# Optimization experiments

Measured on AMD Instinct MI355X. Metric: run time of the kernel, lower is better.

## Reference

```python
import jax, jax.numpy as jnp
import numpy as np

SHIFTS = (1, 2, 4, 8)  # exponential strategy, num_shifts=4

B, L, D = 2, 2048, 2048
CAT = D * (1 + 2 * len(SHIFTS))  # 18432


def setup_inputs() -> dict:
    key = jax.random.key(0)
    kx, kw, kb = jax.random.split(key, 3)
    x = jax.random.normal(kx, (B, L, D), dtype=jnp.float32)
    # nn.Linear(cat_dim, dim_out) weight is [dim_out, cat_dim]; store as [cat_dim, dim_out] transposed for matmul
    W = jax.random.normal(kw, (D, CAT), dtype=jnp.float32) * (1.0 / np.sqrt(CAT))
    b = jax.random.normal(kb, (D,), dtype=jnp.float32) * 0.01
    return {"x": x, "W": W, "b": b}


def reference(x, W, b):
    # x: [B, L, D]; W: [dim_out, cat_dim]; b: [dim_out]
    glo = jnp.mean(x, axis=1, keepdims=True)  # [B, 1, D] global context
    feats = [jax.nn.silu(x)]
    for s in SHIFTS:
        rg = jnp.roll(glo, s, axis=-1)          # [B, 1, D]
        xg = x * rg                              # [B, L, D]
        feats.append(jax.nn.silu(xg))            # inner(s)
        rx = jnp.roll(x, s, axis=-1)
        feats.append(xg - rx * glo)              # wedge(s)
    mixed = jnp.concatenate(feats, axis=-1)      # [B, L, cat_dim]
    out = jnp.einsum('blc,oc->blo', mixed, W) + b
    return out
```

## Files before the change

kernel.cpp:

```cpp
#include <hip/hip_runtime.h>
#include <stdint.h>

#define DDIM 2048
#define LDIM 2048
#define BDIM 2
#define CATK 18432
#define MDIM 4096
#define NDIM 2048
#define KGEMM 12288
#define KCHUNK 6144

typedef short bf16x8 __attribute__((ext_vector_type(8)));
typedef float f32x4 __attribute__((ext_vector_type(4)));
typedef unsigned short u16x8 __attribute__((ext_vector_type(8)));

__device__ __forceinline__ unsigned short f2bf(float f) {
  uint32_t u = __float_as_uint(f);
  return (unsigned short)((u + 0x7fffu + ((u >> 16) & 1u)) >> 16);
}
__device__ __forceinline__ float bf2f(unsigned short h) {
  return __uint_as_float((uint32_t)h << 16);
}
__device__ __forceinline__ float silu_f(float v) { return v / (1.0f + __expf(-v)); }

__device__ __forceinline__ void async16(const void* g, void* l) {
  __builtin_amdgcn_global_load_lds(
      (const __attribute__((address_space(1))) uint32_t*)(uintptr_t)g,
      (__attribute__((address_space(3))) uint32_t*)(uintptr_t)l, 16, 0, 0);
}

__global__ __launch_bounds__(256) void glo_partial(const float* __restrict__ x,
                                                   float* __restrict__ part) {
  int g = blockIdx.x;
  int dc = g & 7, sl = (g >> 3) & 15, b = g >> 7;
  int d = dc * 256 + threadIdx.x;
  const float* p = x + ((size_t)b * LDIM + (size_t)sl * 128) * DDIM + d;
  float s = 0.f;
  #pragma unroll 8
  for (int i = 0; i < 128; ++i) s += p[(size_t)i * DDIM];
  part[(size_t)(b * 16 + sl) * DDIM + d] = s;
}

__global__ __launch_bounds__(256) void glo_final(const float* __restrict__ part,
                                                 float* __restrict__ glo) {
  int idx = blockIdx.x * 256 + threadIdx.x;
  int b = idx >> 11, d = idx & 2047;
  float s = 0.f;
  #pragma unroll
  for (int i = 0; i < 16; ++i) s += part[(size_t)(b * 16 + i) * DDIM + d];
  glo[idx] = s * (1.0f / (float)LDIM);
}

__global__ __launch_bounds__(256) void conv_wB(const float* __restrict__ W,
                                               unsigned short* __restrict__ B0,
                                               unsigned short* __restrict__ B1) {
  int k = blockIdx.x;
  int o = blockIdx.y;
  int srcb = (k == 0) ? 0 : (k == 1) ? 1 : (k == 2) ? 3 : (k == 3) ? 5 : 7;
  const float* src = W + (size_t)o * CATK + srcb * 2048 + threadIdx.x * 8;
  f32x4 a = *(const f32x4*)src;
  f32x4 c = *(const f32x4*)(src + 4);
  u16x8 v;
  v[0] = f2bf(a[0]); v[1] = f2bf(a[1]); v[2] = f2bf(a[2]); v[3] = f2bf(a[3]);
  v[4] = f2bf(c[0]); v[5] = f2bf(c[1]); v[6] = f2bf(c[2]); v[7] = f2bf(c[3]);
  if (k < 3) {
    *(u16x8*)(B0 + (size_t)o * KCHUNK + k * 2048 + threadIdx.x * 8) = v;
  } else {
    size_t d = (size_t)o * KCHUNK + (size_t)(k - 3) * 2048 + threadIdx.x * 8;
    *(u16x8*)(B1 + d) = v;
    *(u16x8*)(B1 + (size_t)2048 * KCHUNK + d) = v;
  }
}

__global__ __launch_bounds__(256) void fold_w(const float* __restrict__ W,
                                              const float* __restrict__ glo,
                                              unsigned short* __restrict__ B1) {
  __shared__ float ws[4][2048];
  __shared__ float g2[2][2048];
  int o = blockIdx.x;
  for (int i = threadIdx.x; i < 512; i += 256) {
    *(f32x4*)&g2[0][i * 4] = *(const f32x4*)&glo[i * 4];
    *(f32x4*)&g2[1][i * 4] = *(const f32x4*)&glo[2048 + i * 4];
    #pragma unroll
    for (int j = 0; j < 4; ++j)
      *(f32x4*)&ws[j][i * 4] =
          *(const f32x4*)(W + (size_t)o * CATK + (2 + 2 * j) * 2048 + i * 4);
  }
  __syncthreads();
  int d0 = threadIdx.x * 8;
  #pragma unroll
  for (int b = 0; b < 2; ++b) {
    u16x8 outv;
    #pragma unroll
    for (int e = 0; e < 8; ++e) {
      int d = d0 + e;
      float v = 0.f;
      #pragma unroll
      for (int j = 0; j < 4; ++j) {
        int s = 1 << j;
        int dm = (d - s) & 2047, dp = (d + s) & 2047;
        v += ws[j][d] * g2[b][dm] - ws[j][dp] * g2[b][dp];
      }
      outv[e] = f2bf(v);
    }
    *(u16x8*)(B1 + (size_t)b * 2048 * KCHUNK + (size_t)o * KCHUNK + 4096 + d0) = outv;
  }
}

__global__ __launch_bounds__(256) void build_mixed(const float* __restrict__ x,
                                                   const float* __restrict__ glo,
                                                   unsigned short* __restrict__ mixed) {
  __shared__ float xs[DDIM];
  __shared__ float gs[DDIM];
  int row = blockIdx.x;
  int b = row >> 11;
  const float* xr = x + (size_t)row * DDIM;
  const float* gr = glo + (size_t)b * DDIM;
  for (int i = threadIdx.x; i < DDIM / 4; i += 256) {
    *(f32x4*)&xs[i * 4] = *(const f32x4*)&xr[i * 4];
    *(f32x4*)&gs[i * 4] = *(const f32x4*)&gr[i * 4];
  }
  __syncthreads();
  unsigned short* mr = mixed + (size_t)row * KGEMM;
  int d0 = threadIdx.x * 8;
  u16x8 o0, oi[4], xb;
  #pragma unroll
  for (int j = 0; j < 8; ++j) {
    int d = d0 + j;
    float xv = xs[d];
    o0[j] = f2bf(silu_f(xv));
    xb[j] = f2bf(xv);
    #pragma unroll
    for (int si = 0; si < 4; ++si) {
      int s = 1 << si;
      int dm = (d - s) & (DDIM - 1);
      oi[si][j] = f2bf(silu_f(xv * gs[dm]));
    }
  }
  *(u16x8*)(mr + d0) = o0;
  #pragma unroll
  for (int si = 0; si < 4; ++si)
    *(u16x8*)(mr + (size_t)(1 + si) * DDIM + d0) = oi[si];
  *(u16x8*)(mr + (size_t)10240 + d0) = xb;
}

#define BAR() __builtin_amdgcn_s_barrier()
#define SCHEDB() __builtin_amdgcn_sched_barrier(0)
#define WAIT_VM4() asm volatile("s_waitcnt vmcnt(4)" ::: "memory")
#define WAIT_VM0() asm volatile("s_waitcnt vmcnt(0)" ::: "memory")
#define WAIT_LGKM0() asm volatile("s_waitcnt lgkmcnt(0)" ::: "memory")

#define STAGE_A(S, H, KREL)                                            \
  do {                                                                 \
    const unsigned short* g_ = gA + (size_t)((H)*128) * KGEMM + (KREL);\
    unsigned short* l_ = stA + ((S)*2 + (H)) * 8192;                   \
    async16(g_, l_);                                                   \
    async16(g_ + (size_t)8 * KGEMM, l_ + 512);                         \
  } while (0)

#define STAGE_B(S, H, KREL)                                             \
  do {                                                                  \
    const unsigned short* g_ = gB + (size_t)((H)*128) * KCHUNK + (KREL);\
    unsigned short* l_ = stB + ((S)*2 + (H)) * 8192;                    \
    async16(g_, l_);                                                    \
    async16(g_ + (size_t)8 * KCHUNK, l_ + 512);                         \
  } while (0)

#define LOAD_A(S, MH)                                                        \
  do {                                                                       \
    _Pragma("unroll") for (int mi = 0; mi < 4; ++mi) {                       \
      ra[mi][0] = *(const bf16x8*)(pA + (S)*16384 + ((MH)*64 + mi*16)*64 + sl0); \
      ra[mi][1] = *(const bf16x8*)(pA + (S)*16384 + ((MH)*64 + mi*16)*64 + sl1); \
    }                                                                        \
  } while (0)

#define LOAD_B(S, NH, RB)                                                    \
  do {                                                                       \
    _Pragma("unroll") for (int nj = 0; nj < 2; ++nj) {                       \
      RB[nj][0] = *(const bf16x8*)(pB + (S)*16384 + ((NH)*32 + nj*16)*64 + sl0); \
      RB[nj][1] = *(const bf16x8*)(pB + (S)*16384 + ((NH)*32 + nj*16)*64 + sl1); \
    }                                                                        \
  } while (0)

#define MFMA_QUAD(MH, NH, RB)                                                \
  do {                                                                       \
    __builtin_amdgcn_s_setprio(1);                                           \
    _Pragma("unroll") for (int kk = 0; kk < 2; ++kk)                         \
      _Pragma("unroll") for (int mi = 0; mi < 4; ++mi)                       \
        _Pragma("unroll") for (int nj = 0; nj < 2; ++nj)                     \
          acc[(MH)*4 + mi][(NH)*2 + nj] = __builtin_amdgcn_mfma_f32_16x16x32_bf16( \
              ra[mi][kk], RB[nj][kk], acc[(MH)*4 + mi][(NH)*2 + nj], 0, 0, 0);     \
    __builtin_amdgcn_s_setprio(0);                                           \
  } while (0)

__global__ __launch_bounds__(512, 2) void gemm256(const unsigned short* __restrict__ A,
                                                  const unsigned short* __restrict__ B0,
                                                  const unsigned short* __restrict__ B1,
                                                  const float* __restrict__ bias,
                                                  unsigned short* __restrict__ P0,
                                                  unsigned short* __restrict__ P1) {
  extern __shared__ unsigned short lds[];
  unsigned short* ldsA = lds;
  unsigned short* ldsB = lds + 32768;

  int bid = blockIdx.x;
  int swz = (bid & 7) * 32 + (bid >> 3);
  int kc = swz >> 7;
  int rem = swz & 127;
  int mt = rem >> 3, nt = rem & 7;
  size_t kbase = (size_t)kc * KCHUNK;

  int tid = threadIdx.x;
  int wave = tid >> 6, lane = tid & 63;
  int wr = wave >> 2, wcol = wave & 3;
  int lrow = lane & 15, kq = lane >> 4, r3 = lrow & 7;
  int rIn8 = lane >> 3;
  int scOff = ((lane & 7) ^ rIn8) * 8;
  int wv16 = wave * 16;

  const unsigned short* gA = A + (size_t)(mt * 256 + wv16 + rIn8) * KGEMM + kbase + scOff;
  const unsigned short* gBb = kc ? (B1 + (size_t)((mt >= 8) ? 2048 : 0) * KCHUNK) : B0;
  const unsigned short* gB = gBb + (size_t)(nt * 256 + wv16 + rIn8) * KCHUNK + scOff;
  unsigned short* stA = ldsA + wv16 * 64;
  unsigned short* stB = ldsB + wv16 * 64;

  const unsigned short* pA = ldsA + wr * 8192 + lrow * 64;
  const unsigned short* pB = ldsB + (wcol >> 1) * 8192 + ((wcol & 1) * 64 + lrow) * 64;
  int sl0 = (kq ^ r3) * 8, sl1 = ((kq + 4) ^ r3) * 8;

  f32x4 acc[8][4];
  #pragma unroll
  for (int i = 0; i < 8; ++i)
    #pragma unroll
    for (int j = 0; j < 4; ++j) acc[i][j] = (f32x4)0.f;
  bf16x8 ra[4][2], rb0[2][2], rb1[2][2];

  STAGE_B(0, 0, 0); STAGE_B(0, 1, 0);
  STAGE_A(0, 0, 0); STAGE_A(0, 1, 0);
  STAGE_B(1, 0, 64); STAGE_B(1, 1, 64);
  WAIT_VM4(); SCHEDB();
  BAR(); SCHEDB();

  for (int t = 0; t < 47; ++t) {
    size_t k0 = (size_t)t * 128;
    LOAD_A(0, 0); LOAD_B(0, 0, rb0);
    STAGE_A(1, 0, k0 + 64);
    BAR(); WAIT_LGKM0(); SCHEDB();
    MFMA_QUAD(0, 0, rb0);
    SCHEDB(); BAR(); SCHEDB();
    LOAD_B(0, 1, rb1);
    STAGE_A(1, 1, k0 + 64);
    BAR(); WAIT_LGKM0(); SCHEDB();
    MFMA_QUAD(0, 1, rb1);
    SCHEDB(); BAR(); SCHEDB();
    LOAD_A(0, 1);
    STAGE_B(0, 0, k0 + 128);
    BAR(); WAIT_LGKM0(); SCHEDB();
    MFMA_QUAD(1, 1, rb1);
    SCHEDB(); BAR(); SCHEDB();
    STAGE_B(0, 1, k0 + 128);
    BAR(); SCHEDB();
    MFMA_QUAD(1, 0, rb0);
    WAIT_VM4(); SCHEDB(); BAR(); SCHEDB();
    LOAD_A(1, 0); LOAD_B(1, 0, rb0);
    STAGE_A(0, 0, k0 + 128);
    BAR(); WAIT_LGKM0(); SCHEDB();
    MFMA_QUAD(0, 0, rb0);
    SCHEDB(); BAR(); SCHEDB();
    LOAD_B(1, 1, rb1);
    STAGE_A(0, 1, k0 + 128);
    BAR(); WAIT_LGKM0(); SCHEDB();
    MFMA_QUAD(0, 1, rb1);
    SCHEDB(); BAR(); SCHEDB();
    LOAD_A(1, 1);
    STAGE_B(1, 0, k0 + 192);
    BAR(); WAIT_LGKM0(); SCHEDB();
    MFMA_QUAD(1, 1, rb1);
    SCHEDB(); BAR(); SCHEDB();
    STAGE_B(1, 1, k0 + 192);
    BAR(); SCHEDB();
    MFMA_QUAD(1, 0, rb0);
    WAIT_VM4(); SCHEDB(); BAR(); SCHEDB();
  }

  {
    size_t k0 = (size_t)47 * 128;
    LOAD_A(0, 0); LOAD_B(0, 0, rb0);
    STAGE_A(1, 0, k0 + 64);
    BAR(); WAIT_LGKM0(); SCHEDB();
    MFMA_QUAD(0, 0, rb0);
    SCHEDB(); BAR(); SCHEDB();
    LOAD_B(0, 1, rb1);
    STAGE_A(1, 1, k0 + 64);
    BAR(); WAIT_LGKM0(); SCHEDB();
    MFMA_QUAD(0, 1, rb1);
    SCHEDB(); BAR(); SCHEDB();
    LOAD_A(0, 1);
    BAR(); WAIT_LGKM0(); SCHEDB();
    MFMA_QUAD(1, 1, rb1);
    SCHEDB(); BAR(); SCHEDB();
    BAR(); SCHEDB();
    MFMA_QUAD(1, 0, rb0);
    WAIT_VM0(); SCHEDB(); BAR(); SCHEDB();
    LOAD_A(1, 0); LOAD_B(1, 0, rb0);
    BAR(); WAIT_LGKM0(); SCHEDB();
    MFMA_QUAD(0, 0, rb0);
    SCHEDB(); BAR(); SCHEDB();
    LOAD_B(1, 1, rb1);
    BAR(); WAIT_LGKM0(); SCHEDB();
    MFMA_QUAD(0, 1, rb1);
    SCHEDB(); BAR(); SCHEDB();
    LOAD_A(1, 1);
    BAR(); WAIT_LGKM0(); SCHEDB();
    MFMA_QUAD(1, 1, rb1);
    SCHEDB(); BAR(); SCHEDB();
    MFMA_QUAD(1, 0, rb0);
  }

  unsigned short* dst = kc ? P1 : P0;
  float bv[4];
  #pragma unroll
  for (int J = 0; J < 4; ++J)
    bv[J] = kc ? 0.f : bias[nt * 256 + wcol * 64 + J * 16 + lrow];
  #pragma unroll
  for (int I = 0; I < 8; ++I) {
    int row0 = mt * 256 + wr * 128 + I * 16 + kq * 4;
    #pragma unroll
    for (int J = 0; J < 4; ++J) {
      int col = nt * 256 + wcol * 64 + J * 16 + lrow;
      #pragma unroll
      for (int r = 0; r < 4; ++r)
        dst[(size_t)(row0 + r) * NDIM + col] = f2bf(acc[I][J][r] + bv[J]);
    }
  }
}

__global__ __launch_bounds__(256) void combine(float* __restrict__ out,
                                               const unsigned short* __restrict__ p0,
                                               const unsigned short* __restrict__ p1) {
  size_t n = (size_t)MDIM * NDIM / 8;
  size_t stride = (size_t)gridDim.x * 256;
  for (size_t i = (size_t)blockIdx.x * 256 + threadIdx.x; i < n; i += stride) {
    u16x8 a = *(const u16x8*)(p0 + i * 8);
    u16x8 c = *(const u16x8*)(p1 + i * 8);
    f32x4 lo, hi;
    #pragma unroll
    for (int j = 0; j < 4; ++j) {
      lo[j] = bf2f(a[j]) + bf2f(c[j]);
      hi[j] = bf2f(a[j + 4]) + bf2f(c[j + 4]);
    }
    *(f32x4*)(out + i * 8) = lo;
    *(f32x4*)(out + i * 8 + 4) = hi;
  }
}

extern "C" void kernel_launch(void* const* d_in, const int* in_sizes, int n_in,
                              void* d_out, int out_size, void* d_ws, size_t ws_size,
                              hipStream_t stream) {
  const float* x = (const float*)d_in[0];
  const float* W = (const float*)d_in[1];
  const float* b = (const float*)d_in[2];
  float* out = (float*)d_out;

  uint8_t* ws = (uint8_t*)d_ws;
  size_t offB0 = 0;
  size_t szB0 = (size_t)NDIM * KCHUNK * 2;
  size_t offB1 = offB0 + szB0;
  size_t szB1 = (size_t)2 * NDIM * KCHUNK * 2;
  size_t offMx = offB1 + szB1;
  size_t szMx = (size_t)MDIM * KGEMM * 2;
  size_t offGlo = offMx + szMx;
  size_t szGlo = (size_t)BDIM * DDIM * 4;
  size_t offPart = offGlo + szGlo;
  size_t szPart = (size_t)BDIM * 16 * DDIM * 4;
  size_t offP0 = offPart + szPart;
  size_t szP0 = (size_t)MDIM * NDIM * 2;
  size_t offP1 = offP0 + szP0;
  size_t szP1 = (size_t)MDIM * NDIM * 2;
  if (ws_size < offP1 + szP1) return;

  unsigned short* B0 = (unsigned short*)(ws + offB0);
  unsigned short* B1 = (unsigned short*)(ws + offB1);
  unsigned short* Mx = (unsigned short*)(ws + offMx);
  float* glo = (float*)(ws + offGlo);
  float* part = (float*)(ws + offPart);
  unsigned short* P0 = (unsigned short*)(ws + offP0);
  unsigned short* P1 = (unsigned short*)(ws + offP1);

  hipFuncSetAttribute((const void*)gemm256, hipFuncAttributeMaxDynamicSharedMemorySize,
                      131072);

  hipLaunchKernelGGL(glo_partial, dim3(256), dim3(256), 0, stream, x, part);
  hipLaunchKernelGGL(glo_final, dim3(16), dim3(256), 0, stream, part, glo);
  hipLaunchKernelGGL(conv_wB, dim3(5, 2048), dim3(256), 0, stream, W, B0, B1);
  hipLaunchKernelGGL(fold_w, dim3(2048), dim3(256), 0, stream, W, glo, B1);
  hipLaunchKernelGGL(build_mixed, dim3(4096), dim3(256), 0, stream, x, glo, Mx);

  hipLaunchKernelGGL(gemm256, dim3(256), dim3(512), 131072, stream, Mx, B0, B1, b, P0, P1);
  hipLaunchKernelGGL(combine, dim3(2048), dim3(256), 0, stream, out, P0, P1);
}
```

Before: 267.2 us.

## Fuse split-K combine into GEMM via cooperative grid sync

Launches the GEMM cooperatively. Blocks holding the second K chunk write bf16 partials, then the whole grid synchronizes, and blocks holding the first K chunk add those partials plus the bias straight into the fp32 output. This removes the separate combine kernel launch and the write and re-read of the P0 partial buffer. In exchange it adds a grid-wide barrier where half the blocks sit idle, and it relies on all 256 blocks being co-resident, falling back to the old path if the cooperative launch fails.

```diff
diff --git a/kernel.cpp b/kernel.cpp
--- a/kernel.cpp
+++ b/kernel.cpp
@@ -1,4 +1,5 @@
 #include <hip/hip_runtime.h>
+#include <hip/hip_cooperative_groups.h>
 #include <stdint.h>
 
 #define DDIM 2048
@@ -198,7 +199,9 @@
                                                   const unsigned short* __restrict__ B1,
                                                   const float* __restrict__ bias,
                                                   unsigned short* __restrict__ P0,
-                                                  unsigned short* __restrict__ P1) {
+                                                  unsigned short* __restrict__ P1,
+                                                  float* __restrict__ out,
+                                                  int coop) {
   extern __shared__ unsigned short lds[];
   unsigned short* ldsA = lds;
   unsigned short* ldsB = lds + 32768;
@@ -317,20 +320,57 @@
     MFMA_QUAD(1, 0, rb0);
   }
 
-  unsigned short* dst = kc ? P1 : P0;
-  float bv[4];
-  #pragma unroll
-  for (int J = 0; J < 4; ++J)
-    bv[J] = kc ? 0.f : bias[nt * 256 + wcol * 64 + J * 16 + lrow];
-  #pragma unroll
-  for (int I = 0; I < 8; ++I) {
-    int row0 = mt * 256 + wr * 128 + I * 16 + kq * 4;
-    #pragma unroll
-    for (int J = 0; J < 4; ++J) {
-      int col = nt * 256 + wcol * 64 + J * 16 + lrow;
+  if (coop) {
+    if (kc) {
       #pragma unroll
-      for (int r = 0; r < 4; ++r)
-        dst[(size_t)(row0 + r) * NDIM + col] = f2bf(acc[I][J][r] + bv[J]);
+      for (int I = 0; I < 8; ++I) {
+        int row0 = mt * 256 + wr * 128 + I * 16 + kq * 4;
+        #pragma unroll
+        for (int J = 0; J < 4; ++J) {
+          int col = nt * 256 + wcol * 64 + J * 16 + lrow;
+          #pragma unroll
+          for (int r = 0; r < 4; ++r)
+            P1[(size_t)(row0 + r) * NDIM + col] = f2bf(acc[I][J][r]);
+        }
+      }
+    }
+    __threadfence();
+    cooperative_groups::this_grid().sync();
+    if (!kc) {
+      float bv[4];
+      #pragma unroll
+      for (int J = 0; J < 4; ++J)
+        bv[J] = bias[nt * 256 + wcol * 64 + J * 16 + lrow];
+      #pragma unroll
+      for (int I = 0; I < 8; ++I) {
+        int row0 = mt * 256 + wr * 128 + I * 16 + kq * 4;
+        #pragma unroll
+        for (int J = 0; J < 4; ++J) {
+          int col = nt * 256 + wcol * 64 + J * 16 + lrow;
+          #pragma unroll
+          for (int r = 0; r < 4; ++r) {
+            size_t idx = (size_t)(row0 + r) * NDIM + col;
+            out[idx] = acc[I][J][r] + bv[J] + bf2f(P1[idx]);
+          }
+        }
+      }
+    }
+  } else {
+    unsigned short* dst = kc ? P1 : P0;
+    float bv[4];
+    #pragma unroll
+    for (int J = 0; J < 4; ++J)
+      bv[J] = kc ? 0.f : bias[nt * 256 + wcol * 64 + J * 16 + lrow];
+    #pragma unroll
+    for (int I = 0; I < 8; ++I) {
+      int row0 = mt * 256 + wr * 128 + I * 16 + kq * 4;
+      #pragma unroll
+      for (int J = 0; J < 4; ++J) {
+        int col = nt * 256 + wcol * 64 + J * 16 + lrow;
+        #pragma unroll
+        for (int r = 0; r < 4; ++r)
+          dst[(size_t)(row0 + r) * NDIM + col] = f2bf(acc[I][J][r] + bv[J]);
+      }
     }
   }
 }
@@ -396,6 +436,18 @@
   hipLaunchKernelGGL(fold_w, dim3(2048), dim3(256), 0, stream, W, glo, B1);
   hipLaunchKernelGGL(build_mixed, dim3(4096), dim3(256), 0, stream, x, glo, Mx);
 
-  hipLaunchKernelGGL(gemm256, dim3(256), dim3(512), 131072, stream, Mx, B0, B1, b, P0, P1);
-  hipLaunchKernelGGL(combine, dim3(2048), dim3(256), 0, stream, out, P0, P1);
-}
+  const unsigned short* Mxc = Mx;
+  const unsigned short* B0c = B0;
+  const unsigned short* B1c = B1;
+  const float* bc = b;
+  int coop = 1;
+  void* args[] = {(void*)&Mxc, (void*)&B0c, (void*)&B1c, (void*)&bc,
+                  (void*)&P0, (void*)&P1, (void*)&out, (void*)&coop};
+  hipError_t ce = hipLaunchCooperativeKernel((void*)gemm256, dim3(256), dim3(512),
+                                             args, 131072, stream);
+  if (ce != hipSuccess) {
+    hipLaunchKernelGGL(gemm256, dim3(256), dim3(512), 131072, stream,
+                       Mx, B0, B1, b, P0, P1, out, 0);
+    hipLaunchKernelGGL(combine, dim3(2048), dim3(256), 0, stream, out, P0, P1);
+  }
+}
```

Result: slower. 385.5 us (+44.2%).
